# Performance work log

Hardware: AMD Instinct MI355X
Metric: run time of the kernel (lower is better)

Reference implementation:

```python
import jax, jax.numpy as jnp
from jax import lax
import numpy as np

NEG = -1e30  # log(0) stand-in, finite for NaN-safe grads


def setup_inputs() -> dict:
    key = jax.random.key(0)
    k1, k2, k3, k4, k5 = jax.random.split(key, 5)
    B, T, U, V = 8, 128, 64, 512
    trans_acts = jax.random.normal(k1, (B, T, V), dtype=jnp.float32)
    pred_acts = jax.random.normal(k2, (B, U + 1, V), dtype=jnp.float32)
    labels = jax.random.randint(k3, (B, U), 1, V, dtype=jnp.int32)  # avoid blank=0
    act_lens = jax.random.randint(k4, (B,), T // 2, T + 1, dtype=jnp.int32)
    label_lens = jax.random.randint(k5, (B,), U // 2, U + 1, dtype=jnp.int32)
    return {"trans_acts": trans_acts, "pred_acts": pred_acts, "labels": labels,
            "act_lens": act_lens, "label_lens": label_lens}


def _rnnt_costs(trans_acts, pred_acts, labels, act_lens, label_lens, blank=0):
    B, T, V = trans_acts.shape
    U1 = pred_acts.shape[1]
    U = U1 - 1
    # joint log-probs: log_softmax(trans[:,t] + pred[:,u]) -> (B, T, U+1, V)
    lp = jax.nn.log_softmax(trans_acts[:, :, None, :] + pred_acts[:, None, :, :], axis=-1)
    blank_lp = lp[..., blank]  # (B, T, U+1)
    # label emission log-probs: lab_lp[b,t,u] = lp[b,t,u,labels[b,u]], u < U
    idx = jnp.broadcast_to(labels[:, None, :, None].astype(jnp.int32), (B, T, U, 1))
    lab_lp = jnp.take_along_axis(lp[:, :, :U, :], idx, axis=3)[..., 0]  # (B,T,U)
    valid_u = jnp.arange(U)[None, :] < label_lens[:, None]               # (B,U)
    lab_lp = jnp.where(valid_u[:, None, :], lab_lp, NEG)

    # alpha DP over the (T x U+1) lattice, scan over t, scan over u
    alpha0 = jnp.concatenate(
        [jnp.zeros((B, 1), lp.dtype), jnp.cumsum(lab_lp[:, 0, :], axis=1)], axis=1)

    def outer(alpha_prev, inp):
        blank_prev, lab_row = inp          # (B,U+1), (B,U)
        a = alpha_prev + blank_prev        # come-from-below term
        def inner(x, ins):                 # x: (B,), left-to-right over u
            a_u, lab_p = ins
            x = jnp.logaddexp(a_u, x + lab_p)
            return x, x
        _, xs = lax.scan(inner, a[:, 0], (a[:, 1:].T, lab_row.T))  # (U,B)
        alpha = jnp.concatenate([a[:, :1], xs.T], axis=1)
        return alpha, alpha

    xs_in = (jnp.swapaxes(blank_lp[:, :-1], 0, 1), jnp.swapaxes(lab_lp[:, 1:], 0, 1))
    _, alphas_rest = lax.scan(outer, alpha0, xs_in)              # (T-1,B,U+1)
    alphas = jnp.concatenate([alpha0[None], alphas_rest], axis=0)  # (T,B,U+1)

    b_idx = jnp.arange(B)
    t_idx = act_lens - 1
    u_idx = label_lens
    ll = alphas[t_idx, b_idx, u_idx] + blank_lp[b_idx, t_idx, u_idx]
    return -ll  # per-example negative log-likelihood


def reference(trans_acts, pred_acts, labels, act_lens, label_lens):
    costs = _rnnt_costs(trans_acts, pred_acts, labels, act_lens, label_lens, blank=0)
    # size_average=False: module returns the batch-summed cost as a 1-element tensor
    return jnp.sum(costs)[None]
```

## Files before the change

kernel.cpp:

```cpp
#include <hip/hip_runtime.h>

#define NEG2 (-30000.0f)
#define L2E  1.4426950408889634f
#define LN2  0.6931471805599453f

constexpr int B = 8, T = 128, U = 64, U1 = 65, V = 512;
constexpr int PDROWS = 200;
constexpr int PDW = PDROWS * 64;

constexpr int ETH_F = 0;
constexpr int EPH_F = ETH_F + (B * T * V) / 2;
constexpr int MT_F  = EPH_F + (B * U1 * V) / 2;
constexpr int MP_F  = MT_F + B * T;
constexpr int T0_F  = MP_F + B * U1;
constexpr int P0_F  = T0_F + B * T;
constexpr int PL_F  = P0_F + B * U1;
constexpr int C0_F  = PL_F + B * U1;
constexpr int TL_F  = C0_F + B * T;
constexpr int PD_F  = TL_F + (B * T * 64) / 2;

typedef _Float16 half_t;
typedef _Float16 v4h __attribute__((ext_vector_type(4)));
typedef _Float16 v8h __attribute__((ext_vector_type(8)));
typedef float    v4f __attribute__((ext_vector_type(4)));

typedef __attribute__((address_space(3))) unsigned int       lds_u32;
typedef const __attribute__((address_space(1))) unsigned int glb_u32;

__device__ __forceinline__ float wave_shr1(float x) {
    int v = __float_as_int(x);
    int r = __builtin_amdgcn_update_dpp(v, v, 0x138, 0xF, 0xF, false);
    return __int_as_float(r);
}

__global__ __launch_bounds__(256) void k_prep(const float* __restrict__ trans,
                                              const float* __restrict__ pred,
                                              const int* __restrict__ labels,
                                              float* __restrict__ ws,
                                              float* __restrict__ out) {
    if (blockIdx.x == 0 && threadIdx.x == 0) out[0] = 0.0f;
    const int wave = (blockIdx.x * blockDim.x + threadIdx.x) >> 6;
    const int lane = threadIdx.x & 63;
    const int nrows_t = B * T;
    const int nrows = nrows_t + B * U1;
    if (wave >= nrows) return;

    const float* src; half_t* dst;
    if (wave < nrows_t) {
        src = trans + (size_t)wave * V;
        dst = (half_t*)(ws + ETH_F) + (size_t)wave * V;
    } else {
        const int r = wave - nrows_t;
        src = pred + (size_t)r * V;
        dst = (half_t*)(ws + EPH_F) + (size_t)r * V;
    }

    const float4 a = ((const float4*)src)[lane];
    const float4 c = ((const float4*)src)[lane + 64];
    float m = fmaxf(fmaxf(fmaxf(a.x, a.y), fmaxf(a.z, a.w)),
                    fmaxf(fmaxf(c.x, c.y), fmaxf(c.z, c.w)));
    #pragma unroll
    for (int off = 32; off >= 1; off >>= 1) m = fmaxf(m, __shfl_xor(m, off));

    v4h h0 = { (half_t)__expf(a.x - m), (half_t)__expf(a.y - m),
               (half_t)__expf(a.z - m), (half_t)__expf(a.w - m) };
    v4h h1 = { (half_t)__expf(c.x - m), (half_t)__expf(c.y - m),
               (half_t)__expf(c.z - m), (half_t)__expf(c.w - m) };
    ((v4h*)dst)[lane]      = h0;
    ((v4h*)dst)[lane + 64] = h1;

    if (wave < nrows_t) {
        const int b = wave >> 7;
        const int lbl = labels[b * U + lane];
        ((half_t*)(ws + TL_F))[(size_t)wave * 64 + lane] = (half_t)src[lbl];
        if (lane == 0) { ws[MT_F + wave] = m; ws[T0_F + wave] = a.x; }
    } else {
        const int r = wave - nrows_t;
        if (lane == 0) {
            const int b = r / U1, u = r % U1;
            ws[MP_F + r] = m; ws[P0_F + r] = a.x;
            if (u < U) ws[PL_F + r] = src[labels[b * U + u]];
        }
    }
}

__global__ __launch_bounds__(64) void k_joint(const int* __restrict__ label_lens,
                                              float* __restrict__ ws) {
    const int lane = threadIdx.x & 63;
    const int wid = blockIdx.x;
    const int b = wid / 40, r = wid % 40;
    const int t0 = (r / 5) * 16, u0 = (r % 5) * 16;
    const int n = lane & 15, q = lane >> 4;

    const v8h* A  = (const v8h*)((const half_t*)(ws + ETH_F) + ((size_t)(b * T + t0 + n)) * V);
    const int  uc = (u0 + n <= 64) ? (u0 + n) : 64;
    const v8h* Bp = (const v8h*)((const half_t*)(ws + EPH_F) + ((size_t)(b * U1 + uc)) * V);

    v4f acc = {0.f, 0.f, 0.f, 0.f};
    #pragma unroll
    for (int c = 0; c < 64; c += 4)
        acc = __builtin_amdgcn_mfma_f32_16x16x32_f16(A[c + q], Bp[c + q], acc, 0, 0, 0);

    const int u = u0 + n;
    if (u > 64) return;
    const int ul = label_lens[b];
    const float mp_u = ws[MP_F + b * U1 + u];
    const float pr0  = ws[P0_F + b * U1 + u];
    const bool has_lab = (u < 64);
    const float prl = has_lab ? ws[PL_F + b * U1 + u] : 0.f;
    half_t* PdH = (half_t*)((uint*)(ws + PD_F) + (size_t)b * PDW);
    const half_t* TLh = (const half_t*)(ws + TL_F) + (size_t)(b * T) * 64;

    #pragma unroll
    for (int i = 0; i < 4; ++i) {
        const int t = t0 + q * 4 + i;
        const float mt = ws[MT_F + b * T + t];
        const float lse2 = (mt + mp_u) * L2E + __log2f(acc[i]);
        const float bl2 = (ws[T0_F + b * T + t] + pr0) * L2E - lse2;
        const int d = t + u + 1;
        if (u >= 1) PdH[(d * 64 + (u - 1)) * 2] = (half_t)bl2;
        else        ws[C0_F + b * T + t] = bl2;
        if (has_lab) {
            const float lb2 = (u >= ul) ? NEG2
                             : ((float)TLh[t * 64 + u] + prl) * L2E - lse2;
            PdH[(d * 64 + u) * 2 + 1] = (half_t)lb2;
        }
    }
}

__global__ __launch_bounds__(64) void k_dp(const float* __restrict__ ws,
                                           const int* __restrict__ act_lens,
                                           const int* __restrict__ label_lens,
                                           float* __restrict__ out) {
    const int b = blockIdx.x, l = threadIdx.x;

    constexpr int DROWS = 192;
    __shared__ __align__(16) uint Pds[DROWS * 64];
    __shared__ float af[T];

    {
        const uint* gsrc = (const uint*)(ws + PD_F) + (size_t)b * PDW + 64;
        #pragma unroll
        for (int i = 0; i < DROWS / 4; ++i)
            __builtin_amdgcn_global_load_lds((glb_u32*)(gsrc + i * 256 + l * 4),
                                             (lds_u32*)(Pds + i * 256), 16, 0, 0);
    }

    const float* c0 = ws + C0_F + b * T;
    float x0 = c0[l], x1 = c0[64 + l];
    #pragma unroll
    for (int off = 1; off < 64; off <<= 1) { float y = __shfl_up(x0, off); if (l >= off) x0 += y; }
    #pragma unroll
    for (int off = 1; off < 64; off <<= 1) { float y = __shfl_up(x1, off); if (l >= off) x1 += y; }
    const float tot = __shfl(x0, 63);
    if (l == 0) af[0] = 0.0f;
    af[l + 1] = x0;
    if (l < 63) af[65 + l] = tot + x1;
    __syncthreads();

    const int tl = act_lens[b] - 1;
    const int ul = label_lens[b];
    const int dmax = tl + ul;

    uint wb[4]; float ab[4];
    #pragma unroll
    for (int j = 0; j < 4; ++j) { wb[j] = Pds[j * 64 + l]; ab[j] = af[j]; }

    float cur = 0.0f;
    #pragma unroll
    for (int d = 1; d <= DROWS; ++d) {
        const int j = (d - 1) & 3;
        const uint w = wb[j];
        const float a00 = ab[j];
        const int pr = (d + 3 < DROWS) ? d + 3 : DROWS - 1;
        wb[j] = Pds[pr * 64 + l];
        ab[j] = af[(d + 3 < T) ? d + 3 : T - 1];

        const int t = d - l - 1;
        union { uint u; half_t h[2]; } cv; cv.u = w;
        const float bn = (float)cv.h[0];
        const float lb = (float)cv.h[1];

        const float sh = wave_shr1(cur);
        const float lv = (l == 0) ? a00 : sh;
        const float a2 = lv + lb;
        const float a1 = (t >= 1) ? cur + bn : NEG2;
        const float mx = fmaxf(a1, a2);
        const float nc = mx + __log2f(1.0f + exp2f(-fabsf(a1 - a2)));
        cur = ((t >= 0) && (t <= tl)) ? nc : cur;
    }

    if (l == ul - 1) {
        union { uint u; half_t h[2]; } cv; cv.u = Pds[dmax * 64 + (ul - 1)];
        atomicAdd(out, -((cur + (float)cv.h[0]) * LN2));
    }
}

extern "C" void kernel_launch(void* const* d_in, const int* in_sizes, int n_in,
                              void* d_out, int out_size, void* d_ws, size_t ws_size,
                              hipStream_t stream) {
    const float* trans      = (const float*)d_in[0];
    const float* pred       = (const float*)d_in[1];
    const int*   labels     = (const int*)d_in[2];
    const int*   act_lens   = (const int*)d_in[3];
    const int*   label_lens = (const int*)d_in[4];
    float* ws  = (float*)d_ws;
    float* out = (float*)d_out;

    const int nrows = B * T + B * U1;
    k_prep<<<(nrows + 3) / 4, 256, 0, stream>>>(trans, pred, labels, ws, out);
    k_joint<<<320, 64, 0, stream>>>(label_lens, ws);
    k_dp<<<8, 64, 0, stream>>>(ws, act_lens, label_lens, out);
}
```

Baseline: 83.48 us.

## Fuse joint MFMA and alpha DP into one per-batch kernel via LDS lattice

The separate joint and DP kernels are merged into one kernel with a 512-thread block per batch. Eight waves compute the joint log-probs with MFMA and write the lattice directly into shared memory, after which wave 0 runs the diagonal DP. This removes the global round-trip of the lattice and one kernel launch. In exchange the joint work drops from 320 blocks to 8, so far fewer CUs are in use and each wave serially covers 5 u-tiles.

```diff
diff --git a/kernel.cpp b/kernel.cpp
--- a/kernel.cpp
+++ b/kernel.cpp
@@ -5,8 +5,6 @@
 #define LN2  0.6931471805599453f
 
 constexpr int B = 8, T = 128, U = 64, U1 = 65, V = 512;
-constexpr int PDROWS = 200;
-constexpr int PDW = PDROWS * 64;
 
 constexpr int ETH_F = 0;
 constexpr int EPH_F = ETH_F + (B * T * V) / 2;
@@ -15,17 +13,12 @@
 constexpr int T0_F  = MP_F + B * U1;
 constexpr int P0_F  = T0_F + B * T;
 constexpr int PL_F  = P0_F + B * U1;
-constexpr int C0_F  = PL_F + B * U1;
-constexpr int TL_F  = C0_F + B * T;
-constexpr int PD_F  = TL_F + (B * T * 64) / 2;
+constexpr int TL_F  = PL_F + B * U1;
 
 typedef _Float16 half_t;
 typedef _Float16 v4h __attribute__((ext_vector_type(4)));
 typedef _Float16 v8h __attribute__((ext_vector_type(8)));
 typedef float    v4f __attribute__((ext_vector_type(4)));
-
-typedef __attribute__((address_space(3))) unsigned int       lds_u32;
-typedef const __attribute__((address_space(1))) unsigned int glb_u32;
 
 __device__ __forceinline__ float wave_shr1(float x) {
     int v = __float_as_int(x);
@@ -84,70 +77,77 @@
     }
 }
 
-__global__ __launch_bounds__(64) void k_joint(const int* __restrict__ label_lens,
-                                              float* __restrict__ ws) {
+__global__ __launch_bounds__(512) void k_joint_dp(const int* __restrict__ label_lens,
+                                                  const int* __restrict__ act_lens,
+                                                  const float* __restrict__ ws,
+                                                  float* __restrict__ out) {
+    const int b = blockIdx.x;
+    const int w = threadIdx.x >> 6;
     const int lane = threadIdx.x & 63;
-    const int wid = blockIdx.x;
-    const int b = wid / 40, r = wid % 40;
-    const int t0 = (r / 5) * 16, u0 = (r % 5) * 16;
     const int n = lane & 15, q = lane >> 4;
 
-    const v8h* A  = (const v8h*)((const half_t*)(ws + ETH_F) + ((size_t)(b * T + t0 + n)) * V);
-    const int  uc = (u0 + n <= 64) ? (u0 + n) : 64;
-    const v8h* Bp = (const v8h*)((const half_t*)(ws + EPH_F) + ((size_t)(b * U1 + uc)) * V);
-
-    v4f acc = {0.f, 0.f, 0.f, 0.f};
-    #pragma unroll
-    for (int c = 0; c < 64; c += 4)
-        acc = __builtin_amdgcn_mfma_f32_16x16x32_f16(A[c + q], Bp[c + q], acc, 0, 0, 0);
-
-    const int u = u0 + n;
-    if (u > 64) return;
+    constexpr int LROWS = 193;
+    __shared__ __align__(16) uint Lat[LROWS * 64];
+    __shared__ float c0s[T];
+    __shared__ float af[T];
+
+    const int t0 = w * 16;
     const int ul = label_lens[b];
-    const float mp_u = ws[MP_F + b * U1 + u];
-    const float pr0  = ws[P0_F + b * U1 + u];
-    const bool has_lab = (u < 64);
-    const float prl = has_lab ? ws[PL_F + b * U1 + u] : 0.f;
-    half_t* PdH = (half_t*)((uint*)(ws + PD_F) + (size_t)b * PDW);
-    const half_t* TLh = (const half_t*)(ws + TL_F) + (size_t)(b * T) * 64;
-
+
+    const v8h* Arow = (const v8h*)((const half_t*)(ws + ETH_F) + ((size_t)(b * T + t0 + n)) * V);
+    v8h a_frag[16];
+    #pragma unroll
+    for (int c = 0; c < 16; ++c) a_frag[c] = Arow[c * 4 + q];
+
+    float mt_i[4], t0v[4];
     #pragma unroll
     for (int i = 0; i < 4; ++i) {
         const int t = t0 + q * 4 + i;
-        const float mt = ws[MT_F + b * T + t];
-        const float lse2 = (mt + mp_u) * L2E + __log2f(acc[i]);
-        const float bl2 = (ws[T0_F + b * T + t] + pr0) * L2E - lse2;
-        const int d = t + u + 1;
-        if (u >= 1) PdH[(d * 64 + (u - 1)) * 2] = (half_t)bl2;
-        else        ws[C0_F + b * T + t] = bl2;
-        if (has_lab) {
-            const float lb2 = (u >= ul) ? NEG2
-                             : ((float)TLh[t * 64 + u] + prl) * L2E - lse2;
-            PdH[(d * 64 + u) * 2 + 1] = (half_t)lb2;
+        mt_i[i] = ws[MT_F + b * T + t];
+        t0v[i]  = ws[T0_F + b * T + t];
+    }
+    const half_t* TLh = (const half_t*)(ws + TL_F) + (size_t)(b * T) * 64;
+    half_t* LatH = (half_t*)Lat;
+
+    #pragma unroll 1
+    for (int j = 0; j < 5; ++j) {
+        const int u0 = j * 16;
+        const int uc = (u0 + n <= 64) ? (u0 + n) : 64;
+        const v8h* Brow = (const v8h*)((const half_t*)(ws + EPH_F) + ((size_t)(b * U1 + uc)) * V);
+
+        v4f acc = {0.f, 0.f, 0.f, 0.f};
+        #pragma unroll
+        for (int c = 0; c < 16; ++c)
+            acc = __builtin_amdgcn_mfma_f32_16x16x32_f16(a_frag[c], Brow[c * 4 + q], acc, 0, 0, 0);
+
+        const int u = u0 + n;
+        if (u <= 64) {
+            const float mp_u = ws[MP_F + b * U1 + u];
+            const float pr0  = ws[P0_F + b * U1 + u];
+            const bool has_lab = (u < 64);
+            const float prl = has_lab ? ws[PL_F + b * U1 + u] : 0.f;
+            #pragma unroll
+            for (int i = 0; i < 4; ++i) {
+                const int t = t0 + q * 4 + i;
+                const float lse2 = (mt_i[i] + mp_u) * L2E + __log2f(acc[i]);
+                const float bl2 = (t0v[i] + pr0) * L2E - lse2;
+                const int d = t + u + 1;
+                if (u >= 1) LatH[(d * 64 + (u - 1)) * 2] = (half_t)bl2;
+                else        c0s[t] = bl2;
+                if (has_lab) {
+                    const float lb2 = (u >= ul) ? NEG2
+                                     : ((float)TLh[t * 64 + u] + prl) * L2E - lse2;
+                    LatH[(d * 64 + u) * 2 + 1] = (half_t)lb2;
+                }
+            }
         }
     }
-}
-
-__global__ __launch_bounds__(64) void k_dp(const float* __restrict__ ws,
-                                           const int* __restrict__ act_lens,
-                                           const int* __restrict__ label_lens,
-                                           float* __restrict__ out) {
-    const int b = blockIdx.x, l = threadIdx.x;
-
-    constexpr int DROWS = 192;
-    __shared__ __align__(16) uint Pds[DROWS * 64];
-    __shared__ float af[T];
-
-    {
-        const uint* gsrc = (const uint*)(ws + PD_F) + (size_t)b * PDW + 64;
-        #pragma unroll
-        for (int i = 0; i < DROWS / 4; ++i)
-            __builtin_amdgcn_global_load_lds((glb_u32*)(gsrc + i * 256 + l * 4),
-                                             (lds_u32*)(Pds + i * 256), 16, 0, 0);
-    }
-
-    const float* c0 = ws + C0_F + b * T;
-    float x0 = c0[l], x1 = c0[64 + l];
+    __syncthreads();
+    if (w != 0) return;
+
+    const int l = lane;
+
+    float x0 = c0s[l], x1 = c0s[64 + l];
     #pragma unroll
     for (int off = 1; off < 64; off <<= 1) { float y = __shfl_up(x0, off); if (l >= off) x0 += y; }
     #pragma unroll
@@ -156,28 +156,26 @@
     if (l == 0) af[0] = 0.0f;
     af[l + 1] = x0;
     if (l < 63) af[65 + l] = tot + x1;
-    __syncthreads();
 
     const int tl = act_lens[b] - 1;
-    const int ul = label_lens[b];
-    const int dmax = tl + ul;
+    const int dmaxp1 = tl + ul + 1;
 
     uint wb[4]; float ab[4];
     #pragma unroll
-    for (int j = 0; j < 4; ++j) { wb[j] = Pds[j * 64 + l]; ab[j] = af[j]; }
+    for (int jj = 0; jj < 4; ++jj) { wb[jj] = Lat[(jj + 1) * 64 + l]; ab[jj] = af[jj]; }
 
     float cur = 0.0f;
     #pragma unroll
-    for (int d = 1; d <= DROWS; ++d) {
-        const int j = (d - 1) & 3;
-        const uint w = wb[j];
-        const float a00 = ab[j];
-        const int pr = (d + 3 < DROWS) ? d + 3 : DROWS - 1;
-        wb[j] = Pds[pr * 64 + l];
-        ab[j] = af[(d + 3 < T) ? d + 3 : T - 1];
+    for (int d = 1; d <= 192; ++d) {
+        const int jj = (d - 1) & 3;
+        const uint wv = wb[jj];
+        const float a00 = ab[jj];
+        const int pr = (d + 4 < LROWS) ? d + 4 : LROWS - 1;
+        wb[jj] = Lat[pr * 64 + l];
+        ab[jj] = af[(d + 3 < T) ? d + 3 : T - 1];
 
         const int t = d - l - 1;
-        union { uint u; half_t h[2]; } cv; cv.u = w;
+        union { uint u; half_t h[2]; } cv; cv.u = wv;
         const float bn = (float)cv.h[0];
         const float lb = (float)cv.h[1];
 
@@ -191,7 +189,7 @@
     }
 
     if (l == ul - 1) {
-        union { uint u; half_t h[2]; } cv; cv.u = Pds[dmax * 64 + (ul - 1)];
+        union { uint u; half_t h[2]; } cv; cv.u = Lat[dmaxp1 * 64 + (ul - 1)];
         atomicAdd(out, -((cur + (float)cv.h[0]) * LN2));
     }
 }
@@ -209,6 +207,5 @@
 
     const int nrows = B * T + B * U1;
     k_prep<<<(nrows + 3) / 4, 256, 0, stream>>>(trans, pred, labels, ws, out);
-    k_joint<<<320, 64, 0, stream>>>(label_lens, ws);
-    k_dp<<<8, 64, 0, stream>>>(ws, act_lens, label_lens, out);
-}
+    k_joint_dp<<<8, 512, 0, stream>>>(label_lens, act_lens, ws, out);
+}
```

New measurement: 102.2 us. 22.4% more time.
